# Optimization experiments

Measured on AMD Instinct MI355X. Metric: run time of the kernel, lower is better.

## Reference

```python
import jax, jax.numpy as jnp
import numpy as np

EPS = 1e-12
B, C, H, M, E, P = 2, 20000, 64, 8, 200000, 3


def setup_inputs() -> dict:
    key = jax.random.key(0)
    ks = jax.random.split(key, 24)
    inp = {}
    inp["features"] = jax.random.normal(ks[0], (B, C, H), jnp.float32)
    inp["positions"] = jax.random.normal(ks[1], (B, C, P), jnp.float32)
    inp["edge_index"] = jax.random.randint(ks[2], (2, E), 0, C)
    inp["degree"] = jax.random.randint(ks[3], (C,), 1, 33).astype(jnp.float32)
    inp["cell_node_indices"] = jax.random.randint(ks[4], (C, M), 0, C)
    mask = (jax.random.uniform(ks[5], (C, M)) > 0.3).astype(jnp.float32)
    inp["cell_node_mask"] = mask.at[:, 0].set(1.0)  # first node always valid (pad semantics)

    def lin(k, fan_in, fan_out):
        return (jax.random.normal(k, (fan_in, fan_out), jnp.float32) / np.sqrt(fan_in)).astype(jnp.float32)

    # message MLP: Linear(2H+4 -> H), SiLU, Linear(H -> H)
    inp["W1"] = lin(ks[6], 2 * H + 4, H); inp["b1"] = jnp.zeros((H,), jnp.float32)
    inp["W2"] = lin(ks[7], H, H);         inp["b2"] = jnp.zeros((H,), jnp.float32)
    # position MLP: Linear(H -> H), SiLU, Linear(H -> 1)
    inp["P1"] = lin(ks[8], H, H);  inp["pb1"] = jnp.zeros((H,), jnp.float32)
    inp["P2"] = lin(ks[9], H, 1);  inp["pb2"] = jnp.zeros((1,), jnp.float32)
    # update MLP: Linear(2H -> H), SiLU, Linear(H -> H)
    inp["U1"] = lin(ks[10], 2 * H, H); inp["ub1"] = jnp.zeros((H,), jnp.float32)
    inp["U2"] = lin(ks[11], H, H);     inp["ub2"] = jnp.zeros((H,), jnp.float32)
    return inp


def _mlp(x, Wa, ba, Wb, bb):
    return jax.nn.silu(x @ Wa + ba) @ Wb + bb


def _forward(features, positions, edge_index, degree, cell_node_indices, cell_node_mask,
             W1, b1, W2, b2, P1, pb1, P2, pb2, U1, ub1, U2, ub2):
    src, dst = edge_index[0], edge_index[1]
    # gather padded node positions per cell: [B, C, M, P]
    node_pos = positions[:, cell_node_indices]

    h_src = features[:, src]                      # [B,E,H]
    h_dst = features[:, dst]
    rel = positions[:, src] - positions[:, dst]   # [B,E,P]
    dist = jnp.linalg.norm(rel, axis=-1, keepdims=True)  # [B,E,1]

    sp = node_pos[:, src]                         # [B,E,M,P]
    dp = node_pos[:, dst]
    mx = cell_node_mask[src]                      # [E,M]
    my = cell_node_mask[dst]

    # pairwise distances [B,E,M,M] via gram trick (avoids [B,E,M,M,P] intermediate)
    sp2 = jnp.sum(sp * sp, -1)                    # [B,E,M]
    dp2 = jnp.sum(dp * dp, -1)
    cross = jnp.einsum('bemp,benp->bemn', sp, dp)
    d = jnp.sqrt(jnp.maximum(sp2[..., :, None] + dp2[..., None, :] - 2.0 * cross, 0.0) + EPS)

    # masked pairwise-distance sum
    w = mx[:, :, None] * my[:, None, :]           # [E,M,M]
    pairwise = jnp.sum(d * w[None], axis=(-1, -2))  # [B,E]

    # centroid distance
    denx = jnp.maximum(mx.sum(-1, keepdims=True), EPS)  # [E,1]
    deny = jnp.maximum(my.sum(-1, keepdims=True), EPS)
    cx = jnp.sum(sp * mx[None, :, :, None], axis=2) / denx[None]  # [B,E,P]
    cy = jnp.sum(dp * my[None, :, :, None], axis=2) / deny[None]
    centroid = jnp.linalg.norm(cx - cy, axis=-1)  # [B,E]

    # Hausdorff distance (masked min/max)
    inf = jnp.float32(jnp.inf)
    d_xy = jnp.where(my[None, :, None, :] <= 0, inf, d)
    min_xy = jnp.where(mx[None] <= 0, 0.0, d_xy.min(-1))  # [B,E,M]
    h_xy = min_xy.max(-1)                                  # [B,E]
    d_yx = jnp.where(mx[None, :, None, :] <= 0, inf, jnp.swapaxes(d, -1, -2))
    min_yx = jnp.where(my[None] <= 0, 0.0, d_yx.min(-1))
    h_yx = min_yx.max(-1)
    haus = jnp.maximum(h_xy, h_yx)

    invariants = jnp.concatenate([dist, pairwise[..., None], centroid[..., None], haus[..., None]], -1)  # [B,E,4]
    msg_in = jnp.concatenate([h_src, h_dst, invariants], -1)  # [B,E,2H+4]
    messages = _mlp(msg_in, W1, b1, W2, b2)                   # [B,E,H]

    # scatter-aggregate into destination cells, degree-normalize
    agg = jnp.zeros_like(features).at[:, dst].add(messages)
    agg = agg / jnp.maximum(degree, 1.0)[None, :, None]

    # position update
    wts = jnp.tanh(_mlp(messages, P1, pb1, P2, pb2))          # [B,E,1]
    pos_upd = jnp.zeros_like(positions).at[:, dst].add(wts * rel)

    new_features = features + _mlp(jnp.concatenate([features, agg], -1), U1, ub1, U2, ub2)
    new_positions = positions + pos_upd
    return new_features, new_positions


def reference(features, positions, edge_index, degree, cell_node_indices, cell_node_mask,
              W1, b1, W2, b2, P1, pb1, P2, pb2, U1, ub1, U2, ub2):
    return _forward(features, positions, edge_index, degree, cell_node_indices, cell_node_mask,
                    W1, b1, W2, b2, P1, pb1, P2, pb2, U1, ub1, U2, ub2)
```

## Files before the change

kernel.cpp:

```cpp
#include <hip/hip_runtime.h>
#include <hip/hip_bf16.h>

#define B_ 2
#define C_ 20000
#define H_ 64
#define M_ 8
#define E_ 200000
#define P_ 3
#define EPS_ 1e-12f
#define ET_ (E_ / 64)

typedef __attribute__((ext_vector_type(8))) short short8;
typedef __attribute__((ext_vector_type(4))) float float4v;

__device__ __forceinline__ float silu_(float x) {
    return x / (1.f + __expf(-x));
}
__device__ __forceinline__ unsigned short f2b(float f) {
    unsigned u = __float_as_uint(f);
    unsigned r = (u + 0x7FFF + ((u >> 16) & 1)) >> 16;
    return (unsigned short)r;
}
__device__ __forceinline__ float b2f(unsigned short h) {
    return __uint_as_float(((unsigned)h) << 16);
}
__device__ __forceinline__ unsigned pk2u(float a, float b) {
    __hip_bfloat162 h = __float22bfloat162_rn(make_float2(a, b));
    unsigned u; __builtin_memcpy(&u, &h, sizeof(u)); return u;
}

#define W1S_OFF 0
#define W2S_OFF 8192
#define P1S_OFF 12288
#define U1S_OFF 16384
#define U2S_OFF 24576
#define WBUF_ELEMS 28672

__global__ __launch_bounds__(256) void prep_kernel(
    const float* __restrict__ W1, const float* __restrict__ W2,
    const float* __restrict__ P1, const float* __restrict__ U1,
    const float* __restrict__ U2, unsigned short* __restrict__ wbuf)
{
    int t = blockIdx.x * 256 + threadIdx.x;
    if (t >= WBUF_ELEMS) return;
    const float* W; int e;
    if (t < W2S_OFF)      { W = W1; e = t; }
    else if (t < U1S_OFF) { W = (t < P1S_OFF) ? W2 : P1; e = (t < P1S_OFF) ? t - W2S_OFF : t - P1S_OFF; }
    else if (t < U2S_OFF) { W = U1; e = t - U1S_OFF; }
    else                  { W = U2; e = t - U2S_OFF; }
    int j = e & 7, lane = (e >> 3) & 63, nt = (e >> 9) & 3, kk = e >> 11;
    int k = kk * 32 + ((lane >> 4) * 8) + j;
    int n = nt * 16 + (lane & 15);
    wbuf[t] = f2b(W[k * 64 + n]);
}

__global__ __launch_bounds__(256) void hist_kernel(
    const int* __restrict__ ei, int* __restrict__ cnt)
{
    int e = blockIdx.x * 256 + threadIdx.x;
    if (e >= E_) return;
    atomicAdd(&cnt[ei[E_ + e]], 1);
}

__global__ __launch_bounds__(256) void alloc_kernel(
    const int* __restrict__ cnt, int* __restrict__ off,
    int* __restrict__ cursor, int* __restrict__ total)
{
    int idx = blockIdx.x * 256 + threadIdx.x;
    int lane = threadIdx.x & 63;
    int v = (idx < C_) ? cnt[idx] : 0;
    int inc = v;
    #pragma unroll
    for (int s = 1; s < 64; s <<= 1) {
        int n = __shfl_up(inc, s);
        if (lane >= s) inc += n;
    }
    int wtot = __shfl(inc, 63);
    int base = 0;
    if (lane == 0) base = atomicAdd(total, wtot);
    base = __shfl(base, 0);
    if (idx < C_) {
        int o = base + inc - v;
        off[idx] = o;
        cursor[idx] = o;
    }
}

__global__ __launch_bounds__(256) void scatter_kernel(
    const int* __restrict__ ei, int* __restrict__ cursor,
    int* __restrict__ ssrc, int* __restrict__ sdst)
{
    int e = blockIdx.x * 256 + threadIdx.x;
    if (e >= E_) return;
    int s = ei[e], d = ei[E_ + e];
    int slot = atomicAdd(&cursor[d], 1);
    ssrc[slot] = s;
    sdst[slot] = d;
}

__global__ __launch_bounds__(256) void desc_kernel(
    const float* __restrict__ pos, const int* __restrict__ cni,
    const float* __restrict__ mask, float* __restrict__ desc)
{
    int tid = blockIdx.x * 256 + threadIdx.x;
    if (tid >= B_ * C_) return;
    int b = tid / C_, c = tid - b * C_;
    const float* pb = pos + (size_t)b * C_ * P_;
    float4* D = (float4*)(desc + (size_t)tid * 40);
    int4 n0 = *(const int4*)&cni[c*8];
    int4 n1 = *(const int4*)&cni[c*8 + 4];
    float4 m0 = *(const float4*)&mask[c*8];
    float4 m1 = *(const float4*)&mask[c*8 + 4];
    int ni[8] = {n0.x, n0.y, n0.z, n0.w, n1.x, n1.y, n1.z, n1.w};
    float mm[8] = {m0.x, m0.y, m0.z, m0.w, m1.x, m1.y, m1.z, m1.w};
    float sx = 0.f, sy = 0.f, sz = 0.f, sm = 0.f;
    #pragma unroll
    for (int m = 0; m < 8; ++m) {
        float x = pb[ni[m]*3+0], y = pb[ni[m]*3+1], z = pb[ni[m]*3+2];
        D[m] = make_float4(x, y, z, mm[m]);
        sx += x * mm[m]; sy += y * mm[m]; sz += z * mm[m]; sm += mm[m];
    }
    float inv = 1.f / fmaxf(sm, EPS_);
    D[8] = make_float4(sx * inv, sy * inv, sz * inv, sm);
    D[9] = make_float4(pb[c*3+0], pb[c*3+1], pb[c*3+2], 0.f);
}

__global__ __launch_bounds__(256) void edge_kernel(
    const float* __restrict__ feat,
    const int* __restrict__ ssrc, const int* __restrict__ sdst,
    const float* __restrict__ desc,
    const unsigned short* __restrict__ wbuf, const float* __restrict__ W1,
    const float* __restrict__ b1, const float* __restrict__ b2,
    const float* __restrict__ pb1, const float* __restrict__ P2,
    const float* __restrict__ pb2,
    unsigned short* __restrict__ Msort, float* __restrict__ wts)
{
    __shared__ unsigned short lds[4 * 3328];

    const int tid  = threadIdx.x;
    const int w    = tid >> 6;
    const int lane = tid & 63;
    const int q    = lane >> 4;
    const int l16  = lane & 15;

    const int tile = blockIdx.x;
    const int b    = tile / ET_;
    const int i0   = (tile - b * ET_) * 64;
    const int s_l  = ssrc[i0 + lane];
    const int d_l  = sdst[i0 + lane];
    const float* fb = feat + (size_t)b * C_ * H_;

    unsigned short* Xw = lds + w * 3328;
    unsigned short* Hw = Xw + 2176;
    unsigned short* Mw = Xw;

    const int sg = __shfl(s_l, w*16 + l16);
    const int dg = __shfl(d_l, w*16 + l16);
    const float4* Ds = (const float4*)(desc + ((size_t)b * C_ + sg) * 40);
    const float4* Dd = (const float4*)(desc + ((size_t)b * C_ + dg) * 40);

    float4 S[8];
    float sp2[8], rowmin[8];
    const float INFV = __builtin_inff();
    #pragma unroll
    for (int i = 0; i < 8; ++i) {
        S[i] = Ds[i];
        sp2[i] = S[i].x*S[i].x + S[i].y*S[i].y + S[i].z*S[i].z;
        rowmin[i] = INFV;
    }
    float pair = 0.f, hyx = 0.f;
    #pragma unroll
    for (int jj = 0; jj < 2; ++jj) {
        float4 Dj = Dd[q*2 + jj];
        float dp2 = Dj.x*Dj.x + Dj.y*Dj.y + Dj.z*Dj.z;
        float colmin = INFV;
        #pragma unroll
        for (int i = 0; i < 8; ++i) {
            float cr = S[i].x*Dj.x + S[i].y*Dj.y + S[i].z*Dj.z;
            float dd = sqrtf(fmaxf(sp2[i] + dp2 - 2.f*cr, 0.f) + EPS_);
            pair += dd * S[i].w * Dj.w;
            rowmin[i] = (Dj.w  > 0.f) ? fminf(rowmin[i], dd) : rowmin[i];
            colmin    = (S[i].w > 0.f) ? fminf(colmin, dd)    : colmin;
        }
        hyx = fmaxf(hyx, (Dj.w > 0.f) ? colmin : 0.f);
    }
    pair += __shfl_xor(pair, 16);  pair += __shfl_xor(pair, 32);
    hyx = fmaxf(hyx, __shfl_xor(hyx, 16));  hyx = fmaxf(hyx, __shfl_xor(hyx, 32));
    #pragma unroll
    for (int i = 0; i < 8; ++i) {
        rowmin[i] = fminf(rowmin[i], __shfl_xor(rowmin[i], 16));
        rowmin[i] = fminf(rowmin[i], __shfl_xor(rowmin[i], 32));
    }
    float hxy = 0.f;
    #pragma unroll
    for (int i = 0; i < 8; ++i)
        hxy = fmaxf(hxy, (S[i].w > 0.f) ? rowmin[i] : 0.f);
    float4 Sc = Ds[8], Dc = Dd[8];
    float cdx = Sc.x - Dc.x, cdy = Sc.y - Dc.y, cdz = Sc.z - Dc.z;
    float4 Sp = Ds[9], Dp = Dd[9];
    float pdx = Sp.x - Dp.x, pdy = Sp.y - Dp.y, pdz = Sp.z - Dp.z;
    const float ivx = sqrtf(pdx*pdx + pdy*pdy + pdz*pdz);
    const float ivy = pair;
    const float ivz = sqrtf(cdx*cdx + cdy*cdy + cdz*cdz);
    const float ivw = fmaxf(hxy, hyx);

    const int rr4 = lane >> 4, c4 = lane & 15;
    #pragma unroll
    for (int it = 0; it < 4; ++it) {
        int rloc = it * 4 + rr4;
        int r = w * 16 + rloc;
        int sr = __shfl(s_l, r);
        int dr = __shfl(d_l, r);
        float4 vs = *(const float4*)&fb[(size_t)sr * 64 + c4 * 4];
        float4 vd = *(const float4*)&fb[(size_t)dr * 64 + c4 * 4];
        *(uint2*)&Xw[rloc*136 + c4*4]      = make_uint2(pk2u(vs.x, vs.y), pk2u(vs.z, vs.w));
        *(uint2*)&Xw[rloc*136 + 64 + c4*4] = make_uint2(pk2u(vd.x, vd.y), pk2u(vd.z, vd.w));
    }

    float4v acc[4];
    #pragma unroll
    for (int nt = 0; nt < 4; ++nt) {
        float bv = b1[nt*16 + l16];
        acc[nt] = (float4v){bv, bv, bv, bv};
    }
    #pragma unroll
    for (int kk = 0; kk < 4; ++kk) {
        short8 a = *(const short8*)&Xw[l16*136 + kk*32 + q*8];
        #pragma unroll
        for (int nt = 0; nt < 4; ++nt) {
            short8 bf = *(const short8*)&wbuf[W1S_OFF + (((kk*4 + nt)*64) + lane) * 8];
            acc[nt] = __builtin_amdgcn_mfma_f32_16x16x32_bf16(a, bf, acc[nt], 0, 0, 0);
        }
    }
    float4 iv[4];
    #pragma unroll
    for (int i = 0; i < 4; ++i) {
        int r = q*4 + i;
        iv[i] = make_float4(__shfl(ivx, r), __shfl(ivy, r),
                            __shfl(ivz, r), __shfl(ivw, r));
    }
    #pragma unroll
    for (int nt = 0; nt < 4; ++nt) {
        float wa = W1[128*64 + nt*16 + l16];
        float wb = W1[129*64 + nt*16 + l16];
        float wc = W1[130*64 + nt*16 + l16];
        float wd = W1[131*64 + nt*16 + l16];
        #pragma unroll
        for (int i = 0; i < 4; ++i)
            acc[nt][i] += iv[i].x*wa + iv[i].y*wb + iv[i].z*wc + iv[i].w*wd;
    }
    #pragma unroll
    for (int nt = 0; nt < 4; ++nt)
        #pragma unroll
        for (int i = 0; i < 4; ++i)
            Hw[(q*4 + i)*72 + nt*16 + l16] = f2b(silu_(acc[nt][i]));

    float4v mac[4];
    #pragma unroll
    for (int nt = 0; nt < 4; ++nt) {
        float bv = b2[nt*16 + l16];
        mac[nt] = (float4v){bv, bv, bv, bv};
    }
    #pragma unroll
    for (int kk = 0; kk < 2; ++kk) {
        short8 a = *(const short8*)&Hw[l16*72 + kk*32 + q*8];
        #pragma unroll
        for (int nt = 0; nt < 4; ++nt) {
            short8 bf = *(const short8*)&wbuf[W2S_OFF + (((kk*4 + nt)*64) + lane) * 8];
            mac[nt] = __builtin_amdgcn_mfma_f32_16x16x32_bf16(a, bf, mac[nt], 0, 0, 0);
        }
    }
    #pragma unroll
    for (int nt = 0; nt < 4; ++nt)
        #pragma unroll
        for (int i = 0; i < 4; ++i)
            Mw[(q*4 + i)*72 + nt*16 + l16] = f2b(mac[nt][i]);

    float4v gac[4];
    #pragma unroll
    for (int nt = 0; nt < 4; ++nt) {
        float bv = pb1[nt*16 + l16];
        gac[nt] = (float4v){bv, bv, bv, bv};
    }
    #pragma unroll
    for (int kk = 0; kk < 2; ++kk) {
        short8 a = *(const short8*)&Mw[l16*72 + kk*32 + q*8];
        #pragma unroll
        for (int nt = 0; nt < 4; ++nt) {
            short8 bf = *(const short8*)&wbuf[P1S_OFF + (((kk*4 + nt)*64) + lane) * 8];
            gac[nt] = __builtin_amdgcn_mfma_f32_16x16x32_bf16(a, bf, gac[nt], 0, 0, 0);
        }
    }
    float p2v[4];
    #pragma unroll
    for (int nt = 0; nt < 4; ++nt) p2v[nt] = P2[nt*16 + l16];
    const float pb2v = pb2[0];

    float* wb_ = wts + (size_t)b * E_ + i0;
    #pragma unroll
    for (int i = 0; i < 4; ++i) {
        float p = 0.f;
        #pragma unroll
        for (int nt = 0; nt < 4; ++nt) p += silu_(gac[nt][i]) * p2v[nt];
        p += __shfl_xor(p, 8);
        p += __shfl_xor(p, 4);
        p += __shfl_xor(p, 2);
        p += __shfl_xor(p, 1);
        float wt = tanhf(p + pb2v);
        if (l16 == 0) wb_[w*16 + q*4 + i] = wt;
    }

    unsigned short* Mg = Msort + ((size_t)b * E_ + i0 + w*16) * 64;
    #pragma unroll
    for (int it = 0; it < 4; ++it) {
        int row = it * 4 + rr4;
        uint2 v = *(const uint2*)&Mw[row*72 + c4*4];
        *(uint2*)&Mg[row*64 + c4*4] = v;
    }
}

__global__ __launch_bounds__(256) void agg_kernel(
    const unsigned short* __restrict__ Msort, const int* __restrict__ off,
    const int* __restrict__ cnt, const float* __restrict__ deg,
    unsigned short* __restrict__ aggb)
{
    int wid = (blockIdx.x * 256 + threadIdx.x) >> 6;
    int lane = threadIdx.x & 63;
    if (wid >= B_ * C_) return;
    int b = wid / C_, c = wid - b * C_;
    int j0 = off[c], n = cnt[c];
    const unsigned short* Mb = Msort + ((size_t)b * E_ + j0) * 64;
    float a0 = 0.f, a1 = 0.f;
    int j = 0;
    for (; j + 2 <= n; j += 2) {
        a0 += b2f(Mb[(size_t)j * 64 + lane]);
        a1 += b2f(Mb[(size_t)(j+1) * 64 + lane]);
    }
    if (j < n) a0 += b2f(Mb[(size_t)j * 64 + lane]);
    float sc = 1.f / fmaxf(deg[c], 1.f);
    aggb[(size_t)wid * 64 + lane] = f2b((a0 + a1) * sc);
}

__global__ __launch_bounds__(256) void pos_kernel(
    const float* __restrict__ pos, const int* __restrict__ ssrc,
    const int* __restrict__ off, const int* __restrict__ cnt,
    const float* __restrict__ wts, float* __restrict__ out_pos)
{
    int wid = (blockIdx.x * 256 + threadIdx.x) >> 6;
    int lane = threadIdx.x & 63;
    if (wid >= B_ * C_) return;
    int b = wid / C_, c = wid - b * C_;
    int j0 = off[c], n = cnt[c];
    const float* pb = pos + (size_t)b * C_ * P_;
    float px = pb[c*3+0], py = pb[c*3+1], pz = pb[c*3+2];
    float ax = 0.f, ay = 0.f, az = 0.f;
    const float* wb_ = wts + (size_t)b * E_;
    for (int j = lane; j < n; j += 64) {
        float wt = wb_[j0 + j];
        int s = ssrc[j0 + j];
        ax += wt * (pb[s*3+0] - px);
        ay += wt * (pb[s*3+1] - py);
        az += wt * (pb[s*3+2] - pz);
    }
    #pragma unroll
    for (int s = 32; s >= 1; s >>= 1) {
        ax += __shfl_xor(ax, s);
        ay += __shfl_xor(ay, s);
        az += __shfl_xor(az, s);
    }
    if (lane < 3) {
        float base = (lane == 0) ? px : (lane == 1) ? py : pz;
        float add  = (lane == 0) ? ax : (lane == 1) ? ay : az;
        out_pos[(size_t)wid * 3 + lane] = base + add;
    }
}

__global__ __launch_bounds__(256) void node_kernel(
    const float* __restrict__ feat, const unsigned short* __restrict__ aggb,
    const unsigned short* __restrict__ wbuf,
    const float* __restrict__ ub1, const float* __restrict__ ub2,
    float* __restrict__ out_feat)
{
    __shared__ unsigned short lds[4 * 3328];

    const int tid  = threadIdx.x;
    const int w    = tid >> 6;
    const int lane = tid & 63;
    const int q    = lane >> 4;
    const int l16  = lane & 15;
    const int g0   = blockIdx.x * 64;

    unsigned short* Xw = lds + w * 3328;
    unsigned short* Hw = Xw + 2176;

    const int rr4 = lane >> 4, c4 = lane & 15;
    #pragma unroll
    for (int it = 0; it < 4; ++it) {
        int rloc = it * 4 + rr4;
        int g = g0 + w*16 + rloc;
        float4 vf = *(const float4*)&feat[(size_t)g * 64 + c4 * 4];
        uint2  va = *(const uint2*)&aggb[(size_t)g * 64 + c4 * 4];
        *(uint2*)&Xw[rloc*136 + c4*4]      = make_uint2(pk2u(vf.x, vf.y), pk2u(vf.z, vf.w));
        *(uint2*)&Xw[rloc*136 + 64 + c4*4] = va;
    }

    float4v acc[4];
    #pragma unroll
    for (int nt = 0; nt < 4; ++nt) {
        float bv = ub1[nt*16 + l16];
        acc[nt] = (float4v){bv, bv, bv, bv};
    }
    #pragma unroll
    for (int kk = 0; kk < 4; ++kk) {
        short8 a = *(const short8*)&Xw[l16*136 + kk*32 + q*8];
        #pragma unroll
        for (int nt = 0; nt < 4; ++nt) {
            short8 bf = *(const short8*)&wbuf[U1S_OFF + (((kk*4 + nt)*64) + lane) * 8];
            acc[nt] = __builtin_amdgcn_mfma_f32_16x16x32_bf16(a, bf, acc[nt], 0, 0, 0);
        }
    }
    #pragma unroll
    for (int nt = 0; nt < 4; ++nt)
        #pragma unroll
        for (int i = 0; i < 4; ++i)
            Hw[(q*4 + i)*72 + nt*16 + l16] = f2b(silu_(acc[nt][i]));

    float4v oac[4];
    #pragma unroll
    for (int nt = 0; nt < 4; ++nt) {
        float bv = ub2[nt*16 + l16];
        oac[nt] = (float4v){bv, bv, bv, bv};
    }
    #pragma unroll
    for (int kk = 0; kk < 2; ++kk) {
        short8 a = *(const short8*)&Hw[l16*72 + kk*32 + q*8];
        #pragma unroll
        for (int nt = 0; nt < 4; ++nt) {
            short8 bf = *(const short8*)&wbuf[U2S_OFF + (((kk*4 + nt)*64) + lane) * 8];
            oac[nt] = __builtin_amdgcn_mfma_f32_16x16x32_bf16(a, bf, oac[nt], 0, 0, 0);
        }
    }
    #pragma unroll
    for (int nt = 0; nt < 4; ++nt)
        #pragma unroll
        for (int i = 0; i < 4; ++i) {
            size_t idx = (size_t)(g0 + w*16 + q*4 + i) * 64 + nt*16 + l16;
            out_feat[idx] = feat[idx] + oac[nt][i];
        }
}

extern "C" void kernel_launch(void* const* d_in, const int* in_sizes, int n_in,
                              void* d_out, int out_size, void* d_ws, size_t ws_size,
                              hipStream_t stream) {
    const float* feat = (const float*)d_in[0];
    const float* pos  = (const float*)d_in[1];
    const int*   ei   = (const int*)d_in[2];
    const float* deg  = (const float*)d_in[3];
    const int*   cni  = (const int*)d_in[4];
    const float* mask = (const float*)d_in[5];
    const float* W1   = (const float*)d_in[6];
    const float* b1   = (const float*)d_in[7];
    const float* W2   = (const float*)d_in[8];
    const float* b2   = (const float*)d_in[9];
    const float* P1   = (const float*)d_in[10];
    const float* pb1  = (const float*)d_in[11];
    const float* P2   = (const float*)d_in[12];
    const float* pb2  = (const float*)d_in[13];
    const float* U1   = (const float*)d_in[14];
    const float* ub1  = (const float*)d_in[15];
    const float* U2   = (const float*)d_in[16];
    const float* ub2  = (const float*)d_in[17];

    float* out_feat = (float*)d_out;
    float* out_pos  = out_feat + (size_t)B_ * C_ * H_;

    float* desc = (float*)d_ws;
    float* wts  = desc + (size_t)B_ * C_ * 40;
    unsigned short* wbuf  = (unsigned short*)(wts + (size_t)B_ * E_);
    unsigned short* Msort = wbuf + WBUF_ELEMS;
    unsigned short* aggb  = Msort + (size_t)B_ * E_ * 64;
    int* cnt    = (int*)(aggb + (size_t)B_ * C_ * 64);
    int* total  = cnt + C_;
    int* off    = total + 1;
    int* cursor = off + C_;
    int* ssrc   = cursor + C_;
    int* sdst   = ssrc + E_;

    hipMemsetAsync(cnt, 0, (C_ + 1) * sizeof(int), stream);

    prep_kernel<<<(WBUF_ELEMS + 255) / 256, 256, 0, stream>>>(W1, W2, P1, U1, U2, wbuf);
    hist_kernel<<<(E_ + 255) / 256, 256, 0, stream>>>(ei, cnt);
    desc_kernel<<<(B_ * C_ + 255) / 256, 256, 0, stream>>>(pos, cni, mask, desc);
    alloc_kernel<<<(C_ + 255) / 256, 256, 0, stream>>>(cnt, off, cursor, total);
    scatter_kernel<<<(E_ + 255) / 256, 256, 0, stream>>>(ei, cursor, ssrc, sdst);

    edge_kernel<<<B_ * ET_, 256, 0, stream>>>(
        feat, ssrc, sdst, desc, wbuf, W1, b1, b2, pb1, P2, pb2, Msort, wts);

    agg_kernel<<<(B_ * C_) / 4, 256, 0, stream>>>(Msort, off, cnt, deg, aggb);
    pos_kernel<<<(B_ * C_) / 4, 256, 0, stream>>>(pos, ssrc, off, cnt, wts, out_pos);

    node_kernel<<<(B_ * C_) / 64, 256, 0, stream>>>(
        feat, aggb, wbuf, ub1, ub2, out_feat);
}
```

Before: 247.1 us.

## Fuse aggregation into edge kernel via segmented atomics and pre-convert features to bf16

Merges the prep, histogram and descriptor kernels into one launch, which also converts features to bf16 once so the edge and node kernels gather half the bytes. The edge kernel now reduces its messages and position deltas over runs of equal destination within each wave (edges are sorted by destination) and atomically adds them into a zeroed fp32 aggregate and into a copy of the positions. This removes the bf16 message buffer round trip and the separate agg and pos kernels. In exchange it adds float atomics, which make summation order nondeterministic, plus a memset and a device copy.

```diff
diff --git a/kernel.cpp b/kernel.cpp
--- a/kernel.cpp
+++ b/kernel.cpp
@@ -36,35 +36,69 @@
 #define U2S_OFF 24576
 #define WBUF_ELEMS 28672
 
-__global__ __launch_bounds__(256) void prep_kernel(
+#define NB_PREP  120
+#define NB_FEATB 2500
+#define NB_DESC  157
+#define NB_HIST  782
+#define NB_COMBO (NB_PREP + NB_FEATB + NB_DESC + NB_HIST)
+
+__global__ __launch_bounds__(256) void combo_kernel(
     const float* __restrict__ W1, const float* __restrict__ W2,
     const float* __restrict__ P1, const float* __restrict__ U1,
-    const float* __restrict__ U2, unsigned short* __restrict__ wbuf)
-{
-    int t = blockIdx.x * 256 + threadIdx.x;
-    if (t >= WBUF_ELEMS) return;
-    const float* W; int e;
-    if (t < W2S_OFF)      { W = W1; e = t; }
-    else if (t < U1S_OFF) { W = (t < P1S_OFF) ? W2 : P1; e = (t < P1S_OFF) ? t - W2S_OFF : t - P1S_OFF; }
-    else if (t < U2S_OFF) { W = U1; e = t - U1S_OFF; }
-    else                  { W = U2; e = t - U2S_OFF; }
-    int j = e & 7, lane = (e >> 3) & 63, nt = (e >> 9) & 3, kk = e >> 11;
-    int k = kk * 32 + ((lane >> 4) * 8) + j;
-    int n = nt * 16 + (lane & 15);
-    wbuf[t] = f2b(W[k * 64 + n]);
-}
-
-__global__ __launch_bounds__(256) void hist_kernel(
+    const float* __restrict__ U2, unsigned short* __restrict__ wbuf,
+    const float* __restrict__ feat, unsigned short* __restrict__ featb,
+    const float* __restrict__ pos, const int* __restrict__ cni,
+    const float* __restrict__ mask, float* __restrict__ desc,
     const int* __restrict__ ei, int* __restrict__ cnt)
 {
-    int e = blockIdx.x * 256 + threadIdx.x;
-    if (e >= E_) return;
-    atomicAdd(&cnt[ei[E_ + e]], 1);
+    const int bid = blockIdx.x;
+    if (bid < NB_PREP) {
+        int t = bid * 256 + threadIdx.x;
+        if (t >= WBUF_ELEMS) return;
+        const float* W; int e;
+        if (t < W2S_OFF)      { W = W1; e = t; }
+        else if (t < U1S_OFF) { W = (t < P1S_OFF) ? W2 : P1; e = (t < P1S_OFF) ? t - W2S_OFF : t - P1S_OFF; }
+        else if (t < U2S_OFF) { W = U1; e = t - U1S_OFF; }
+        else                  { W = U2; e = t - U2S_OFF; }
+        int j = e & 7, lane = (e >> 3) & 63, nt = (e >> 9) & 3, kk = e >> 11;
+        int k = kk * 32 + ((lane >> 4) * 8) + j;
+        int n = nt * 16 + (lane & 15);
+        wbuf[t] = f2b(W[k * 64 + n]);
+    } else if (bid < NB_PREP + NB_FEATB) {
+        int t = (bid - NB_PREP) * 256 + threadIdx.x;
+        float4 v = *(const float4*)&feat[(size_t)t * 4];
+        *(uint2*)&featb[(size_t)t * 4] = make_uint2(pk2u(v.x, v.y), pk2u(v.z, v.w));
+    } else if (bid < NB_PREP + NB_FEATB + NB_DESC) {
+        int tid = (bid - NB_PREP - NB_FEATB) * 256 + threadIdx.x;
+        if (tid >= B_ * C_) return;
+        int b = tid / C_, c = tid - b * C_;
+        const float* pb = pos + (size_t)b * C_ * P_;
+        float4* D = (float4*)(desc + (size_t)tid * 40);
+        int4 n0 = *(const int4*)&cni[c*8];
+        int4 n1 = *(const int4*)&cni[c*8 + 4];
+        float4 m0 = *(const float4*)&mask[c*8];
+        float4 m1 = *(const float4*)&mask[c*8 + 4];
+        int ni[8] = {n0.x, n0.y, n0.z, n0.w, n1.x, n1.y, n1.z, n1.w};
+        float mm[8] = {m0.x, m0.y, m0.z, m0.w, m1.x, m1.y, m1.z, m1.w};
+        float sx = 0.f, sy = 0.f, sz = 0.f, sm = 0.f;
+        #pragma unroll
+        for (int m = 0; m < 8; ++m) {
+            float x = pb[ni[m]*3+0], y = pb[ni[m]*3+1], z = pb[ni[m]*3+2];
+            D[m] = make_float4(x, y, z, mm[m]);
+            sx += x * mm[m]; sy += y * mm[m]; sz += z * mm[m]; sm += mm[m];
+        }
+        float inv = 1.f / fmaxf(sm, EPS_);
+        D[8] = make_float4(sx * inv, sy * inv, sz * inv, sm);
+        D[9] = make_float4(pb[c*3+0], pb[c*3+1], pb[c*3+2], 0.f);
+    } else {
+        int e = (bid - NB_PREP - NB_FEATB - NB_DESC) * 256 + threadIdx.x;
+        if (e >= E_) return;
+        atomicAdd(&cnt[ei[E_ + e]], 1);
+    }
 }
 
 __global__ __launch_bounds__(256) void alloc_kernel(
-    const int* __restrict__ cnt, int* __restrict__ off,
-    int* __restrict__ cursor, int* __restrict__ total)
+    const int* __restrict__ cnt, int* __restrict__ cursor, int* __restrict__ total)
 {
     int idx = blockIdx.x * 256 + threadIdx.x;
     int lane = threadIdx.x & 63;
@@ -79,11 +113,7 @@
     int base = 0;
     if (lane == 0) base = atomicAdd(total, wtot);
     base = __shfl(base, 0);
-    if (idx < C_) {
-        int o = base + inc - v;
-        off[idx] = o;
-        cursor[idx] = o;
-    }
+    if (idx < C_) cursor[idx] = base + inc - v;
 }
 
 __global__ __launch_bounds__(256) void scatter_kernel(
@@ -98,42 +128,15 @@
     sdst[slot] = d;
 }
 
-__global__ __launch_bounds__(256) void desc_kernel(
-    const float* __restrict__ pos, const int* __restrict__ cni,
-    const float* __restrict__ mask, float* __restrict__ desc)
-{
-    int tid = blockIdx.x * 256 + threadIdx.x;
-    if (tid >= B_ * C_) return;
-    int b = tid / C_, c = tid - b * C_;
-    const float* pb = pos + (size_t)b * C_ * P_;
-    float4* D = (float4*)(desc + (size_t)tid * 40);
-    int4 n0 = *(const int4*)&cni[c*8];
-    int4 n1 = *(const int4*)&cni[c*8 + 4];
-    float4 m0 = *(const float4*)&mask[c*8];
-    float4 m1 = *(const float4*)&mask[c*8 + 4];
-    int ni[8] = {n0.x, n0.y, n0.z, n0.w, n1.x, n1.y, n1.z, n1.w};
-    float mm[8] = {m0.x, m0.y, m0.z, m0.w, m1.x, m1.y, m1.z, m1.w};
-    float sx = 0.f, sy = 0.f, sz = 0.f, sm = 0.f;
-    #pragma unroll
-    for (int m = 0; m < 8; ++m) {
-        float x = pb[ni[m]*3+0], y = pb[ni[m]*3+1], z = pb[ni[m]*3+2];
-        D[m] = make_float4(x, y, z, mm[m]);
-        sx += x * mm[m]; sy += y * mm[m]; sz += z * mm[m]; sm += mm[m];
-    }
-    float inv = 1.f / fmaxf(sm, EPS_);
-    D[8] = make_float4(sx * inv, sy * inv, sz * inv, sm);
-    D[9] = make_float4(pb[c*3+0], pb[c*3+1], pb[c*3+2], 0.f);
-}
-
 __global__ __launch_bounds__(256) void edge_kernel(
-    const float* __restrict__ feat,
+    const unsigned short* __restrict__ featb,
     const int* __restrict__ ssrc, const int* __restrict__ sdst,
     const float* __restrict__ desc,
     const unsigned short* __restrict__ wbuf, const float* __restrict__ W1,
     const float* __restrict__ b1, const float* __restrict__ b2,
     const float* __restrict__ pb1, const float* __restrict__ P2,
     const float* __restrict__ pb2,
-    unsigned short* __restrict__ Msort, float* __restrict__ wts)
+    float* __restrict__ aggf, float* __restrict__ out_pos)
 {
     __shared__ unsigned short lds[4 * 3328];
 
@@ -142,20 +145,21 @@
     const int lane = tid & 63;
     const int q    = lane >> 4;
     const int l16  = lane & 15;
+    const int w16  = w * 16;
 
     const int tile = blockIdx.x;
     const int b    = tile / ET_;
     const int i0   = (tile - b * ET_) * 64;
     const int s_l  = ssrc[i0 + lane];
     const int d_l  = sdst[i0 + lane];
-    const float* fb = feat + (size_t)b * C_ * H_;
+    const unsigned short* fb = featb + (size_t)b * C_ * H_;
 
     unsigned short* Xw = lds + w * 3328;
     unsigned short* Hw = Xw + 2176;
     unsigned short* Mw = Xw;
 
-    const int sg = __shfl(s_l, w*16 + l16);
-    const int dg = __shfl(d_l, w*16 + l16);
+    const int sg = __shfl(s_l, w16 + l16);
+    const int dg = __shfl(d_l, w16 + l16);
     const float4* Ds = (const float4*)(desc + ((size_t)b * C_ + sg) * 40);
     const float4* Dd = (const float4*)(desc + ((size_t)b * C_ + dg) * 40);
 
@@ -198,8 +202,8 @@
     float4 Sc = Ds[8], Dc = Dd[8];
     float cdx = Sc.x - Dc.x, cdy = Sc.y - Dc.y, cdz = Sc.z - Dc.z;
     float4 Sp = Ds[9], Dp = Dd[9];
-    float pdx = Sp.x - Dp.x, pdy = Sp.y - Dp.y, pdz = Sp.z - Dp.z;
-    const float ivx = sqrtf(pdx*pdx + pdy*pdy + pdz*pdz);
+    const float relx = Sp.x - Dp.x, rely = Sp.y - Dp.y, relz = Sp.z - Dp.z;
+    const float ivx = sqrtf(relx*relx + rely*rely + relz*relz);
     const float ivy = pair;
     const float ivz = sqrtf(cdx*cdx + cdy*cdy + cdz*cdz);
     const float ivw = fmaxf(hxy, hyx);
@@ -208,13 +212,13 @@
     #pragma unroll
     for (int it = 0; it < 4; ++it) {
         int rloc = it * 4 + rr4;
-        int r = w * 16 + rloc;
+        int r = w16 + rloc;
         int sr = __shfl(s_l, r);
         int dr = __shfl(d_l, r);
-        float4 vs = *(const float4*)&fb[(size_t)sr * 64 + c4 * 4];
-        float4 vd = *(const float4*)&fb[(size_t)dr * 64 + c4 * 4];
-        *(uint2*)&Xw[rloc*136 + c4*4]      = make_uint2(pk2u(vs.x, vs.y), pk2u(vs.z, vs.w));
-        *(uint2*)&Xw[rloc*136 + 64 + c4*4] = make_uint2(pk2u(vd.x, vd.y), pk2u(vd.z, vd.w));
+        uint2 vs = *(const uint2*)&fb[(size_t)sr * 64 + c4 * 4];
+        uint2 vd = *(const uint2*)&fb[(size_t)dr * 64 + c4 * 4];
+        *(uint2*)&Xw[rloc*136 + c4*4]      = vs;
+        *(uint2*)&Xw[rloc*136 + 64 + c4*4] = vd;
     }
 
     float4v acc[4];
@@ -296,7 +300,6 @@
     for (int nt = 0; nt < 4; ++nt) p2v[nt] = P2[nt*16 + l16];
     const float pb2v = pb2[0];
 
-    float* wb_ = wts + (size_t)b * E_ + i0;
     #pragma unroll
     for (int i = 0; i < 4; ++i) {
         float p = 0.f;
@@ -307,76 +310,47 @@
         p += __shfl_xor(p, 2);
         p += __shfl_xor(p, 1);
         float wt = tanhf(p + pb2v);
-        if (l16 == 0) wb_[w*16 + q*4 + i] = wt;
-    }
-
-    unsigned short* Mg = Msort + ((size_t)b * E_ + i0 + w*16) * 64;
-    #pragma unroll
-    for (int it = 0; it < 4; ++it) {
-        int row = it * 4 + rr4;
-        uint2 v = *(const uint2*)&Mw[row*72 + c4*4];
-        *(uint2*)&Mg[row*64 + c4*4] = v;
-    }
-}
-
-__global__ __launch_bounds__(256) void agg_kernel(
-    const unsigned short* __restrict__ Msort, const int* __restrict__ off,
-    const int* __restrict__ cnt, const float* __restrict__ deg,
-    unsigned short* __restrict__ aggb)
-{
-    int wid = (blockIdx.x * 256 + threadIdx.x) >> 6;
-    int lane = threadIdx.x & 63;
-    if (wid >= B_ * C_) return;
-    int b = wid / C_, c = wid - b * C_;
-    int j0 = off[c], n = cnt[c];
-    const unsigned short* Mb = Msort + ((size_t)b * E_ + j0) * 64;
-    float a0 = 0.f, a1 = 0.f;
-    int j = 0;
-    for (; j + 2 <= n; j += 2) {
-        a0 += b2f(Mb[(size_t)j * 64 + lane]);
-        a1 += b2f(Mb[(size_t)(j+1) * 64 + lane]);
-    }
-    if (j < n) a0 += b2f(Mb[(size_t)j * 64 + lane]);
-    float sc = 1.f / fmaxf(deg[c], 1.f);
-    aggb[(size_t)wid * 64 + lane] = f2b((a0 + a1) * sc);
-}
-
-__global__ __launch_bounds__(256) void pos_kernel(
-    const float* __restrict__ pos, const int* __restrict__ ssrc,
-    const int* __restrict__ off, const int* __restrict__ cnt,
-    const float* __restrict__ wts, float* __restrict__ out_pos)
-{
-    int wid = (blockIdx.x * 256 + threadIdx.x) >> 6;
-    int lane = threadIdx.x & 63;
-    if (wid >= B_ * C_) return;
-    int b = wid / C_, c = wid - b * C_;
-    int j0 = off[c], n = cnt[c];
-    const float* pb = pos + (size_t)b * C_ * P_;
-    float px = pb[c*3+0], py = pb[c*3+1], pz = pb[c*3+2];
-    float ax = 0.f, ay = 0.f, az = 0.f;
-    const float* wb_ = wts + (size_t)b * E_;
-    for (int j = lane; j < n; j += 64) {
-        float wt = wb_[j0 + j];
-        int s = ssrc[j0 + j];
-        ax += wt * (pb[s*3+0] - px);
-        ay += wt * (pb[s*3+1] - py);
-        az += wt * (pb[s*3+2] - pz);
-    }
-    #pragma unroll
-    for (int s = 32; s >= 1; s >>= 1) {
-        ax += __shfl_xor(ax, s);
-        ay += __shfl_xor(ay, s);
-        az += __shfl_xor(az, s);
-    }
+        if (l16 == 0) *(float*)&Mw[(q*4 + i)*72 + 64] = wt;
+    }
+
+    float mrow[16];
+    #pragma unroll
+    for (int rr = 0; rr < 16; ++rr) mrow[rr] = b2f(Mw[rr*72 + lane]);
+    float wtl = *(const float*)&Mw[l16*72 + 64];
+
+    float* aggB = aggf + (size_t)b * C_ * 64;
+    float* opB  = out_pos + (size_t)b * C_ * 3;
+
+    int dprev = __shfl(d_l, w16);
+    float colacc = 0.f, pxa = 0.f, pya = 0.f, pza = 0.f;
+    #pragma unroll
+    for (int rr = 0; rr < 16; ++rr) {
+        int dcur = __shfl(d_l, w16 + rr);
+        if (dcur != dprev) {
+            atomicAdd(&aggB[(size_t)dprev * 64 + lane], colacc);
+            if (lane < 3) {
+                float v = (lane == 0) ? pxa : (lane == 1) ? pya : pza;
+                atomicAdd(&opB[(size_t)dprev * 3 + lane], v);
+            }
+            colacc = 0.f; pxa = 0.f; pya = 0.f; pza = 0.f;
+            dprev = dcur;
+        }
+        float wt = __shfl(wtl, rr);
+        colacc += mrow[rr];
+        pxa += wt * __shfl(relx, rr);
+        pya += wt * __shfl(rely, rr);
+        pza += wt * __shfl(relz, rr);
+    }
+    atomicAdd(&aggB[(size_t)dprev * 64 + lane], colacc);
     if (lane < 3) {
-        float base = (lane == 0) ? px : (lane == 1) ? py : pz;
-        float add  = (lane == 0) ? ax : (lane == 1) ? ay : az;
-        out_pos[(size_t)wid * 3 + lane] = base + add;
+        float v = (lane == 0) ? pxa : (lane == 1) ? pya : pza;
+        atomicAdd(&opB[(size_t)dprev * 3 + lane], v);
     }
 }
 
 __global__ __launch_bounds__(256) void node_kernel(
-    const float* __restrict__ feat, const unsigned short* __restrict__ aggb,
+    const float* __restrict__ feat, const unsigned short* __restrict__ featb,
+    const float* __restrict__ aggf, const float* __restrict__ deg,
     const unsigned short* __restrict__ wbuf,
     const float* __restrict__ ub1, const float* __restrict__ ub2,
     float* __restrict__ out_feat)
@@ -398,10 +372,13 @@
     for (int it = 0; it < 4; ++it) {
         int rloc = it * 4 + rr4;
         int g = g0 + w*16 + rloc;
-        float4 vf = *(const float4*)&feat[(size_t)g * 64 + c4 * 4];
-        uint2  va = *(const uint2*)&aggb[(size_t)g * 64 + c4 * 4];
-        *(uint2*)&Xw[rloc*136 + c4*4]      = make_uint2(pk2u(vf.x, vf.y), pk2u(vf.z, vf.w));
-        *(uint2*)&Xw[rloc*136 + 64 + c4*4] = va;
+        int gc = (g >= C_) ? g - C_ : g;
+        float sc = 1.f / fmaxf(deg[gc], 1.f);
+        uint2  vf = *(const uint2*)&featb[(size_t)g * 64 + c4 * 4];
+        float4 va = *(const float4*)&aggf[(size_t)g * 64 + c4 * 4];
+        *(uint2*)&Xw[rloc*136 + c4*4]      = vf;
+        *(uint2*)&Xw[rloc*136 + 64 + c4*4] =
+            make_uint2(pk2u(va.x*sc, va.y*sc), pk2u(va.z*sc, va.w*sc));
     }
 
     float4v acc[4];
@@ -475,31 +452,29 @@
     float* out_pos  = out_feat + (size_t)B_ * C_ * H_;
 
     float* desc = (float*)d_ws;
-    float* wts  = desc + (size_t)B_ * C_ * 40;
-    unsigned short* wbuf  = (unsigned short*)(wts + (size_t)B_ * E_);
-    unsigned short* Msort = wbuf + WBUF_ELEMS;
-    unsigned short* aggb  = Msort + (size_t)B_ * E_ * 64;
-    int* cnt    = (int*)(aggb + (size_t)B_ * C_ * 64);
+    float* aggf = desc + (size_t)B_ * C_ * 40;
+    unsigned short* featb = (unsigned short*)(aggf + (size_t)B_ * C_ * 64);
+    unsigned short* wbuf  = featb + (size_t)B_ * C_ * 64;
+    int* cnt    = (int*)(wbuf + WBUF_ELEMS);
     int* total  = cnt + C_;
-    int* off    = total + 1;
-    int* cursor = off + C_;
+    int* cursor = total + 1;
     int* ssrc   = cursor + C_;
     int* sdst   = ssrc + E_;
 
     hipMemsetAsync(cnt, 0, (C_ + 1) * sizeof(int), stream);
-
-    prep_kernel<<<(WBUF_ELEMS + 255) / 256, 256, 0, stream>>>(W1, W2, P1, U1, U2, wbuf);
-    hist_kernel<<<(E_ + 255) / 256, 256, 0, stream>>>(ei, cnt);
-    desc_kernel<<<(B_ * C_ + 255) / 256, 256, 0, stream>>>(pos, cni, mask, desc);
-    alloc_kernel<<<(C_ + 255) / 256, 256, 0, stream>>>(cnt, off, cursor, total);
+    hipMemsetAsync(aggf, 0, (size_t)B_ * C_ * 64 * sizeof(float), stream);
+    hipMemcpyAsync(out_pos, pos, (size_t)B_ * C_ * P_ * sizeof(float),
+                   hipMemcpyDeviceToDevice, stream);
+
+    combo_kernel<<<NB_COMBO, 256, 0, stream>>>(
+        W1, W2, P1, U1, U2, wbuf, feat, featb, pos, cni, mask, desc, ei, cnt);
+
+    alloc_kernel<<<(C_ + 255) / 256, 256, 0, stream>>>(cnt, cursor, total);
     scatter_kernel<<<(E_ + 255) / 256, 256, 0, stream>>>(ei, cursor, ssrc, sdst);
 
     edge_kernel<<<B_ * ET_, 256, 0, stream>>>(
-        feat, ssrc, sdst, desc, wbuf, W1, b1, b2, pb1, P2, pb2, Msort, wts);
-
-    agg_kernel<<<(B_ * C_) / 4, 256, 0, stream>>>(Msort, off, cnt, deg, aggb);
-    pos_kernel<<<(B_ * C_) / 4, 256, 0, stream>>>(pos, ssrc, off, cnt, wts, out_pos);
+        featb, ssrc, sdst, desc, wbuf, W1, b1, b2, pb1, P2, pb2, aggf, out_pos);
 
     node_kernel<<<(B_ * C_) / 64, 256, 0, stream>>>(
-        feat, aggb, wbuf, ub1, ub2, out_feat);
-}
+        feat, featb, aggf, deg, wbuf, ub1, ub2, out_feat);
+}
```

After: 226.5 us. -8.3%, faster.
